# Performance work log

Measured on AMD Instinct MI355X. Metric: run time of the kernel, lower is better.

Reference implementation:

```python
import jax, jax.numpy as jnp
import numpy as np

N_NODES = 50000
N_EDGES = 1_600_000
F_IN = 128
F_OUT = 8
K_TAPS = 4
AVG_DEG = 32.0


def setup_inputs() -> dict:
    key = jax.random.key(0)
    k1, k2, k3, k4, k5 = jax.random.split(key, 5)
    x = jax.random.normal(k1, (N_NODES, F_IN), dtype=jnp.float32)
    gso_rows = jax.random.randint(k2, (N_EDGES,), 0, N_NODES, dtype=jnp.int32)
    gso_cols = jax.random.randint(k3, (N_EDGES,), 0, N_NODES, dtype=jnp.int32)
    gso_vals = jax.random.uniform(k4, (N_EDGES,), dtype=jnp.float32) / AVG_DEG
    # filterCoeff = randn(outFeat, filter_order) * 0.1 as in torch __init__
    coeff = jax.random.normal(k5, (F_OUT, K_TAPS), dtype=jnp.float32) * 0.1
    return {"x": x, "gso_rows": gso_rows, "gso_cols": gso_cols,
            "gso_vals": gso_vals, "coeff": coeff}


def reference(x, gso_rows, gso_cols, gso_vals, coeff):
    # Faithful to the torch code INCLUDING its carried-over SpMV state:
    # output feature o uses powers S^{1+o(K-1)} .. S^{o(K-1)+K} of x.
    F_out, K = coeff.shape
    N = x.shape[0]
    max_power = F_out * (K - 1) + 1  # highest S power needed

    def spmv(Z):  # S @ Z via edge-list gather + segment_sum scatter
        return jax.ops.segment_sum(gso_vals[:, None] * Z[gso_cols], gso_rows,
                                   num_segments=N)

    def step(Z, _):
        Zn = spmv(Z)
        return Zn, Zn.sum(axis=1)  # sum over in-features done up-front

    # s[p-1, n] = sum_f (S^p x)[n, f], for p = 1..max_power
    _, s = jax.lax.scan(step, x, None, length=max_power)  # (max_power, N)

    # power index (0-based into s) used by output o, tap i: o*(K-1) + i
    idx = jnp.arange(F_out)[:, None] * (K - 1) + jnp.arange(K)[None, :]  # (F_out, K)
    sg = s[idx]  # (F_out, K, N)
    y = jnp.einsum('ok,okn->no', coeff, sg)  # (N, F_out)
    return y
```

## Files before the change

### kernel.cpp

```cpp
#include <hip/hip_runtime.h>
#include <hip/hip_bf16.h>

#define N_NODES 50000
#define N_EDGES 1600000
#define F_IN    128
#define F_OUT   8
#define K_TAPS  4
#define MAX_POWER 25

#define NBLK    256
#define NTHR    512
#define RPB     196
#define CHUNK   4096
#define NPART   391
#define ECAP_G  8192
#define ECAP_L  7168
#define NITER   14
#define CSB     800

#define FSTRIDE 16

__device__ inline int wave_incl_scan(int v, int lane) {
    #pragma unroll
    for (int off = 1; off < 64; off <<= 1) {
        int t = __shfl_up(v, off, 64);
        if (lane >= off) v += t;
    }
    return v;
}

__device__ inline void st_coh(float* p, float v) {
    __hip_atomic_store(p, v, __ATOMIC_RELAXED, __HIP_MEMORY_SCOPE_AGENT);
}
__device__ inline void st_coh_i(int* p, int v) {
    __hip_atomic_store(p, v, __ATOMIC_RELAXED, __HIP_MEMORY_SCOPE_AGENT);
}
__device__ inline int ld_coh_i(const int* p) {
    return __hip_atomic_load((int*)p, __ATOMIC_RELAXED, __HIP_MEMORY_SCOPE_AGENT);
}

__global__ void partition_kernel(const int* __restrict__ rows,
                                 const int* __restrict__ cols,
                                 const float* __restrict__ vals,
                                 int* __restrict__ gcnt,
                                 int2* __restrict__ edges, int n_edges) {
    __shared__ int lhist[NBLK];
    __shared__ int lcur[NBLK];
    __shared__ int lbase[NBLK];
    __shared__ int2 stage[CHUNK];
    __shared__ unsigned char sbkt[CHUNK];
    __shared__ int wsum[4];
    int tid = threadIdx.x;
    int base = blockIdx.x * CHUNK;
    int cend = min(base + CHUNK, n_edges);

    lhist[tid] = 0;
    __syncthreads();
    for (int i = base + tid; i < cend; i += 256)
        atomicAdd(&lhist[rows[i] / RPB], 1);
    __syncthreads();

    int lane = tid & 63, wid = tid >> 6;
    int h = lhist[tid];
    int incl = wave_incl_scan(h, lane);
    if (lane == 63) wsum[wid] = incl;
    __syncthreads();
    int woff = 0;
    for (int w = 0; w < wid; ++w) woff += wsum[w];
    int excl = woff + incl - h;
    lcur[tid] = excl;
    if (h) {
        int g = atomicAdd(&gcnt[tid], h);
        lbase[tid] = tid * ECAP_G + g - excl;
    }
    __syncthreads();

    for (int i = base + tid; i < cend; i += 256) {
        int r = rows[i], c = cols[i];
        float v = vals[i];
        int b = r / RPB;
        int pos = atomicAdd(&lcur[b], 1);
        stage[pos] = make_int2(((r - b * RPB) << 16) | c, __float_as_int(v));
        sbkt[pos] = (unsigned char)b;
    }
    __syncthreads();

    int cn = cend - base;
    for (int i = tid; i < cn; i += 256) {
        int b = sbkt[i];
        int o = lbase[b] + i;
        if (o - b * ECAP_G < ECAP_G)
            edges[o] = stage[i];
    }
}

__global__ __launch_bounds__(NTHR, 1)
void chain_kernel(const int* __restrict__ gcnt,
                  const int2* __restrict__ edges,
                  const float* __restrict__ x,
                  const float* __restrict__ coeff,
                  float* __restrict__ u,
                  float* __restrict__ s,
                  float* __restrict__ y,
                  int* __restrict__ flags,
                  int* __restrict__ gen_word,
                  int n_nodes) {
    __shared__ int2  esort[ECAP_L];
    __shared__ int   chist[CSB];
    __shared__ int   ccur[CSB];
    __shared__ int   wsum8[8];
    __shared__ float acc[RPB];
    __shared__ float yacc[RPB * F_OUT];
    __shared__ float lcoeff[F_OUT * K_TAPS];

    int tid = threadIdx.x;
    int b = blockIdx.x;

    if (tid < RPB) acc[tid] = 0.f;
    for (int j = tid; j < RPB * F_OUT; j += NTHR) yacc[j] = 0.f;
    if (tid < F_OUT * K_TAPS) lcoeff[tid] = coeff[tid];

    int cnt = min(gcnt[b], ECAP_G);
    const int2* eb = edges + (size_t)b * ECAP_G;

    for (int i = tid; i < CSB; i += NTHR) chist[i] = 0;
    __syncthreads();
    if (cnt <= ECAP_L) {
        for (int i = tid; i < cnt; i += NTHR) {
            int2 e = eb[i];
            atomicAdd(&chist[(e.x & 0xFFFF) >> 6], 1);
        }
        __syncthreads();
        int lane = tid & 63, wid = tid >> 6;
        int b0 = 2 * tid;
        int h0 = (b0 < CSB) ? chist[b0] : 0;
        int h1 = (b0 + 1 < CSB) ? chist[b0 + 1] : 0;
        int ps = h0 + h1;
        int incl = wave_incl_scan(ps, lane);
        if (lane == 63) wsum8[wid] = incl;
        __syncthreads();
        int woff = 0;
        for (int w = 0; w < wid; ++w) woff += wsum8[w];
        int ex = woff + incl - ps;
        if (b0 < CSB) ccur[b0] = ex;
        if (b0 + 1 < CSB) ccur[b0 + 1] = ex + h0;
        __syncthreads();
        for (int i = tid; i < cnt; i += NTHR) {
            int2 e = eb[i];
            int pos = atomicAdd(&ccur[(e.x & 0xFFFF) >> 6], 1);
            esort[pos] = e;
        }
        __syncthreads();
    } else {
        int cl = min(cnt, ECAP_L);
        for (int i = tid; i < cl; i += NTHR) esort[i] = eb[i];
        __syncthreads();
    }

    int   ecol[NITER];
    int   erow[NITER];
    float eval[NITER];
    int cntl = min(cnt, ECAP_L);
    #pragma unroll
    for (int j = 0; j < NITER; ++j) {
        int idx = tid + j * NTHR;
        int2 e = (idx < cntl) ? esort[idx] : make_int2(0, 0);
        ecol[j] = e.x & 0xFFFF;
        erow[j] = e.x >> 16;
        eval[j] = __int_as_float(e.y);
    }

    {
        int lane = tid & 63;
        int wave = (b * NTHR + tid) >> 6;
        int n_waves = NBLK * 8;
        for (int node = wave; node < n_nodes; node += n_waves) {
            const float2* xp = (const float2*)(x + (size_t)node * F_IN);
            float2 v = xp[lane];
            float sm = v.x + v.y;
            #pragma unroll
            for (int off = 32; off > 0; off >>= 1)
                sm += __shfl_down(sm, off, 64);
            if (lane == 0) st_coh(&u[node], sm);
        }
    }
    __syncthreads();
    if (tid == 0) st_coh_i(&flags[b * FSTRIDE], 1);
    if (b == 0 && tid < NBLK)
        while (ld_coh_i(&flags[tid * FSTRIDE]) < 1) __builtin_amdgcn_s_sleep(1);
    __syncthreads();
    if (b == 0 && tid == 0) st_coh_i(gen_word, 1);
    if (tid == 0)
        while (ld_coh_i(gen_word) < 1) __builtin_amdgcn_s_sleep(1);
    __syncthreads();

    for (int p = 0; p < MAX_POWER; ++p) {
        const float* __restrict__ src = (p == 0) ? u : s + (size_t)(p - 1) * n_nodes;
        float* dst = s + (size_t)p * n_nodes;

        float v[NITER];
        #pragma unroll
        for (int j = 0; j < NITER; ++j) v[j] = src[ecol[j]];
        #pragma unroll
        for (int j = 0; j < NITER; ++j)
            atomicAdd(&acc[erow[j]], eval[j] * v[j]);
        for (int k = ECAP_L + tid; k < cnt; k += NTHR) {
            int2 ev = eb[k];
            atomicAdd(&acc[ev.x >> 16], __int_as_float(ev.y) * src[ev.x & 0xFFFF]);
        }
        __syncthreads();

        float val = (tid < RPB) ? acc[tid] : 0.f;
        int row = b * RPB + tid;
        bool last = (p == MAX_POWER - 1);
        if (!last && tid < RPB && row < n_nodes) st_coh(&dst[row], val);

        if (!last) {
            __syncthreads();
            if (tid == 0) st_coh_i(&flags[b * FSTRIDE], p + 2);
        }
        if (tid < RPB) {
            acc[tid] = 0.f;
            #pragma unroll
            for (int o = 0; o < F_OUT; ++o) {
                int k = p - (K_TAPS - 1) * o;
                if (k >= 0 && k < K_TAPS)
                    yacc[tid * F_OUT + o] += lcoeff[o * K_TAPS + k] * val;
            }
        }
        if (!last) {
            if (b == 0 && tid < NBLK)
                while (ld_coh_i(&flags[tid * FSTRIDE]) < p + 2)
                    __builtin_amdgcn_s_sleep(1);
            __syncthreads();
            if (b == 0 && tid == 0) st_coh_i(gen_word, p + 2);
            if (tid == 0)
                while (ld_coh_i(gen_word) < p + 2) __builtin_amdgcn_s_sleep(1);
            __syncthreads();
        }
    }

    __syncthreads();
    for (int j = tid; j < RPB * F_OUT; j += NTHR) {
        int row = b * RPB + (j >> 3);
        if (row < n_nodes) y[(size_t)row * F_OUT + (j & 7)] = yacc[j];
    }
}

extern "C" void kernel_launch(void* const* d_in, const int* in_sizes, int n_in,
                              void* d_out, int out_size, void* d_ws, size_t ws_size,
                              hipStream_t stream) {
    const float* x        = (const float*)d_in[0];
    const int*   gso_rows = (const int*)d_in[1];
    const int*   gso_cols = (const int*)d_in[2];
    const float* gso_vals = (const float*)d_in[3];
    const float* coeff    = (const float*)d_in[4];
    float* y = (float*)d_out;

    float* u     = (float*)d_ws;
    float* s     = u + N_NODES;
    int2*  edges = (int2*)(s + (size_t)MAX_POWER * N_NODES);
    int*   gcnt  = (int*)(edges + (size_t)NBLK * ECAP_G);
    int*   flags = gcnt + NBLK;
    int*   gen_word = flags + NBLK * FSTRIDE;

    size_t ctrl_ints = (size_t)NBLK + (size_t)NBLK * FSTRIDE + 16;
    hipMemsetAsync(gcnt, 0, ctrl_ints * sizeof(int), stream);

    partition_kernel<<<NPART, 256, 0, stream>>>(
        gso_rows, gso_cols, gso_vals, gcnt, edges, N_EDGES);

    int n_nodes = N_NODES;
    void* args[] = { (void*)&gcnt, (void*)&edges, (void*)&x, (void*)&coeff,
                     (void*)&u, (void*)&s, (void*)&y, (void*)&flags,
                     (void*)&gen_word, (void*)&n_nodes };
    hipLaunchCooperativeKernel((void*)chain_kernel, dim3(NBLK), dim3(NTHR),
                               args, 0, stream);
}
```

Before: 491.0 us.

## Replace two-level grid barrier with all-block flag polling and hoist rowsum

The per-power grid barrier no longer has block 0 gather flags and then broadcast a generation word. Every block now polls all 256 block flags directly, which removes one round trip of latency at each of the 24 barriers. The input row-sum moves into a separate kernel launched before the cooperative kernel, which removes the initial barrier. A per-block float4 prefetch of a slice of the source vector is also added to warm L2 before the gathers. The risks are heavier polling traffic on the flag array and one extra kernel launch.

```diff
diff --git a/kernel.cpp b/kernel.cpp
--- a/kernel.cpp
+++ b/kernel.cpp
@@ -19,6 +19,7 @@
 #define CSB     800
 
 #define FSTRIDE 16
+#define PF_LEN  1600
 
 __device__ inline int wave_incl_scan(int v, int lane) {
     #pragma unroll
@@ -37,6 +38,21 @@
 }
 __device__ inline int ld_coh_i(const int* p) {
     return __hip_atomic_load((int*)p, __ATOMIC_RELAXED, __HIP_MEMORY_SCOPE_AGENT);
+}
+
+__global__ void rowsum_kernel(const float* __restrict__ x,
+                              float* __restrict__ u, int n_nodes) {
+    int wave_in_block = threadIdx.x >> 6;
+    int lane = threadIdx.x & 63;
+    int node = blockIdx.x * 4 + wave_in_block;
+    if (node >= n_nodes) return;
+    const float2* xp = (const float2*)(x + (size_t)node * F_IN);
+    float2 v = xp[lane];
+    float s = v.x + v.y;
+    #pragma unroll
+    for (int off = 32; off > 0; off >>= 1)
+        s += __shfl_down(s, off, 64);
+    if (lane == 0) u[node] = s;
 }
 
 __global__ void partition_kernel(const int* __restrict__ rows,
@@ -97,13 +113,11 @@
 __global__ __launch_bounds__(NTHR, 1)
 void chain_kernel(const int* __restrict__ gcnt,
                   const int2* __restrict__ edges,
-                  const float* __restrict__ x,
                   const float* __restrict__ coeff,
-                  float* __restrict__ u,
+                  const float* __restrict__ u,
                   float* __restrict__ s,
                   float* __restrict__ y,
                   int* __restrict__ flags,
-                  int* __restrict__ gen_word,
                   int n_nodes) {
     __shared__ int2  esort[ECAP_L];
     __shared__ int   chist[CSB];
@@ -170,33 +184,18 @@
         eval[j] = __int_as_float(e.y);
     }
 
-    {
-        int lane = tid & 63;
-        int wave = (b * NTHR + tid) >> 6;
-        int n_waves = NBLK * 8;
-        for (int node = wave; node < n_nodes; node += n_waves) {
-            const float2* xp = (const float2*)(x + (size_t)node * F_IN);
-            float2 v = xp[lane];
-            float sm = v.x + v.y;
-            #pragma unroll
-            for (int off = 32; off > 0; off >>= 1)
-                sm += __shfl_down(sm, off, 64);
-            if (lane == 0) st_coh(&u[node], sm);
-        }
-    }
-    __syncthreads();
-    if (tid == 0) st_coh_i(&flags[b * FSTRIDE], 1);
-    if (b == 0 && tid < NBLK)
-        while (ld_coh_i(&flags[tid * FSTRIDE]) < 1) __builtin_amdgcn_s_sleep(1);
-    __syncthreads();
-    if (b == 0 && tid == 0) st_coh_i(gen_word, 1);
-    if (tid == 0)
-        while (ld_coh_i(gen_word) < 1) __builtin_amdgcn_s_sleep(1);
-    __syncthreads();
+    int slice = (b >> 3) & 31;
+    int pf_base = slice * PF_LEN + (tid << 2);
+    bool pf_on = (tid < (PF_LEN >> 2));
 
     for (int p = 0; p < MAX_POWER; ++p) {
         const float* __restrict__ src = (p == 0) ? u : s + (size_t)(p - 1) * n_nodes;
         float* dst = s + (size_t)p * n_nodes;
+
+        if (pf_on && pf_base + 3 < n_nodes) {
+            float4 pf = *(const float4*)(src + pf_base);
+            asm volatile("" :: "v"(pf.x), "v"(pf.y), "v"(pf.z), "v"(pf.w));
+        }
 
         float v[NITER];
         #pragma unroll
@@ -217,7 +216,7 @@
 
         if (!last) {
             __syncthreads();
-            if (tid == 0) st_coh_i(&flags[b * FSTRIDE], p + 2);
+            if (tid == 0) st_coh_i(&flags[b * FSTRIDE], p + 1);
         }
         if (tid < RPB) {
             acc[tid] = 0.f;
@@ -229,13 +228,9 @@
             }
         }
         if (!last) {
-            if (b == 0 && tid < NBLK)
-                while (ld_coh_i(&flags[tid * FSTRIDE]) < p + 2)
+            if (tid < NBLK)
+                while (ld_coh_i(&flags[tid * FSTRIDE]) < p + 1)
                     __builtin_amdgcn_s_sleep(1);
-            __syncthreads();
-            if (b == 0 && tid == 0) st_coh_i(gen_word, p + 2);
-            if (tid == 0)
-                while (ld_coh_i(gen_word) < p + 2) __builtin_amdgcn_s_sleep(1);
             __syncthreads();
         }
     }
@@ -262,18 +257,19 @@
     int2*  edges = (int2*)(s + (size_t)MAX_POWER * N_NODES);
     int*   gcnt  = (int*)(edges + (size_t)NBLK * ECAP_G);
     int*   flags = gcnt + NBLK;
-    int*   gen_word = flags + NBLK * FSTRIDE;
-
-    size_t ctrl_ints = (size_t)NBLK + (size_t)NBLK * FSTRIDE + 16;
+
+    size_t ctrl_ints = (size_t)NBLK + (size_t)NBLK * FSTRIDE;
     hipMemsetAsync(gcnt, 0, ctrl_ints * sizeof(int), stream);
 
     partition_kernel<<<NPART, 256, 0, stream>>>(
         gso_rows, gso_cols, gso_vals, gcnt, edges, N_EDGES);
 
+    rowsum_kernel<<<(N_NODES + 3) / 4, 256, 0, stream>>>(x, u, N_NODES);
+
     int n_nodes = N_NODES;
-    void* args[] = { (void*)&gcnt, (void*)&edges, (void*)&x, (void*)&coeff,
+    void* args[] = { (void*)&gcnt, (void*)&edges, (void*)&coeff,
                      (void*)&u, (void*)&s, (void*)&y, (void*)&flags,
-                     (void*)&gen_word, (void*)&n_nodes };
+                     (void*)&n_nodes };
     hipLaunchCooperativeKernel((void*)chain_kernel, dim3(NBLK), dim3(NTHR),
                                args, 0, stream);
 }
```

Result: faster. 475.0 us (-3.3%).
